# Kernel tuning notes

Hardware: AMD Instinct MI355X
Metric: run time of the kernel (lower is better)

The kernel has to match this reference:

```python
import jax, jax.numpy as jnp
import numpy as np

LN_EPS = 1e-5

def _layernorm(x, g, b):
    mu = jnp.mean(x, axis=-1, keepdims=True)
    var = jnp.var(x, axis=-1, keepdims=True)
    return (x - mu) * jax.lax.rsqrt(var + LN_EPS) * g + b

def setup_inputs() -> dict:
    key = jax.random.key(0)
    ks = jax.random.split(key, 8)
    B, N, n, m, a = 4096, 50000, 1024, 16384, 256
    return {
        "x": jax.random.normal(ks[0], (B, n), dtype=jnp.float32),
        "X_data": jax.random.normal(ks[1], (N, n), dtype=jnp.float32),
        "memory_indices": jax.random.randint(ks[2], (m,), 0, N, dtype=jnp.int64)
            if jax.config.jax_enable_x64 else jax.random.randint(ks[2], (m,), 0, N, dtype=jnp.int32),
        "W_q": jax.random.normal(ks[3], (a, n), dtype=jnp.float32) / np.sqrt(n),
        "W_k": jax.random.normal(ks[4], (a, n), dtype=jnp.float32) / np.sqrt(n),
        "W_v": jax.random.normal(ks[5], (n, n), dtype=jnp.float32) / np.sqrt(n),
        "g_q": jnp.ones((a,), jnp.float32), "b_q": jnp.zeros((a,), jnp.float32),
        "g_k": jnp.ones((a,), jnp.float32), "b_k": jnp.zeros((a,), jnp.float32),
        "g_v": jnp.ones((n,), jnp.float32), "b_v": jnp.zeros((n,), jnp.float32),
    }

def reference(x, X_data, memory_indices, W_q, W_k, W_v, g_q, b_q, g_k, b_k, g_v, b_v):
    # Gather memory bank rows: [m, n]
    X_cross = X_data[memory_indices]
    n = x.shape[-1]
    # preprocess(): scalar normalizer so mean row norm ~= sqrt(n) (SAE convention)
    C = jnp.mean(jnp.linalg.norm(X_cross, axis=-1)) / jnp.sqrt(jnp.asarray(n, x.dtype))
    X_cross = X_cross / C
    xs = x / C
    # QKV projections (Linear, no bias) + per-stream LayerNorm
    q = _layernorm(xs @ W_q.T, g_q, b_q)        # [B, a]
    k = _layernorm(X_cross @ W_k.T, g_k, b_k)   # [m, a]
    v = _layernorm(X_cross @ W_v.T, g_v, b_v)   # [m, n]
    # scaled dot-product attention over the memory bank
    scale = 1.0 / np.sqrt(q.shape[-1])
    attn = jax.nn.softmax(jnp.einsum('ba,ma->bm', q, k) * scale, axis=-1)  # [B, m]
    x_hat = attn @ v                             # [B, n]
    return (xs, x_hat, attn, v)
```

## Files before the change

### kernel.cpp

```cpp
#include <hip/hip_runtime.h>
#include <math.h>

typedef _Float16 hlf4 __attribute__((ext_vector_type(4)));
typedef _Float16 hlf8 __attribute__((ext_vector_type(8)));
typedef float f32x4 __attribute__((ext_vector_type(4)));

static __device__ __forceinline__ void gl_lds16(const void* g, void* l) {
    __builtin_amdgcn_global_load_lds(
        (const __attribute__((address_space(1))) unsigned int*)g,
        (__attribute__((address_space(3))) unsigned int*)l, 16, 0, 0);
}

static __device__ __forceinline__ float blk_sum(float v) {
    __shared__ float sm[256];
    int tid = threadIdx.x;
    sm[tid] = v; __syncthreads();
#pragma unroll
    for (int s = 128; s > 0; s >>= 1) {
        if (tid < s) sm[tid] += sm[tid + s];
        __syncthreads();
    }
    float r = sm[0]; __syncthreads();
    return r;
}

static __device__ __forceinline__ float blk_max(float v) {
    __shared__ float sm[256];
    int tid = threadIdx.x;
    sm[tid] = v; __syncthreads();
#pragma unroll
    for (int s = 128; s > 0; s >>= 1) {
        if (tid < s) sm[tid] = fmaxf(sm[tid], sm[tid + s]);
        __syncthreads();
    }
    float r = sm[0]; __syncthreads();
    return r;
}

__global__ __launch_bounds__(256) void k_cinv(
    const float* __restrict__ norms, int m, int n, float* __restrict__ cinv) {
    float s = 0.f;
    for (int i = threadIdx.x; i < m; i += 256) s += norms[i];
    float tot = blk_sum(s);
    if (threadIdx.x == 0) cinv[0] = (float)m * sqrtf((float)n) / tot;
}

__global__ __launch_bounds__(256) void k_scale2(
    const float* __restrict__ x, const float* __restrict__ cinv,
    float* __restrict__ y, _Float16* __restrict__ yh, long long total4) {
    float c = cinv[0];
    long long i = blockIdx.x * 256ll + threadIdx.x;
    long long stride = (long long)gridDim.x * 256ll;
    for (; i < total4; i += stride) {
        float4 v = ((const float4*)x)[i];
        float4 w = {v.x * c, v.y * c, v.z * c, v.w * c};
        ((float4*)y)[i] = w;
        hlf4 o = {(_Float16)v.x, (_Float16)v.y, (_Float16)v.z, (_Float16)v.w};
        ((hlf4*)yh)[i] = o;
    }
}

__global__ __launch_bounds__(256) void k_gather_cvt(
    const float* __restrict__ X, const int* __restrict__ idx,
    _Float16* __restrict__ out, float* __restrict__ norms, int n) {
    long long r = idx[blockIdx.x];
    const float* src = X + r * (long long)n;
    _Float16* dst = out + (long long)blockIdx.x * n;
    float s = 0.f;
    for (int k = threadIdx.x * 4; k < n; k += 256 * 4) {
        float4 v = *(const float4*)(src + k);
        hlf4 o = {(_Float16)v.x, (_Float16)v.y, (_Float16)v.z, (_Float16)v.w};
        *(hlf4*)(dst + k) = o;
        s = fmaf(v.x, v.x, s); s = fmaf(v.y, v.y, s);
        s = fmaf(v.z, v.z, s); s = fmaf(v.w, v.w, s);
    }
    float tot = blk_sum(s);
    if (threadIdx.x == 0) norms[blockIdx.x] = sqrtf(tot);
}

__global__ __launch_bounds__(256) void k_cvt(
    const float* __restrict__ in, _Float16* __restrict__ out, long long n4,
    float sc) {
    long long i = blockIdx.x * 256ll + threadIdx.x;
    long long stride = (long long)gridDim.x * 256ll;
    for (; i < n4; i += stride) {
        float4 v = ((const float4*)in)[i];
        hlf4 o = {(_Float16)(v.x * sc), (_Float16)(v.y * sc),
                  (_Float16)(v.z * sc), (_Float16)(v.w * sc)};
        ((hlf4*)out)[i] = o;
    }
}

__global__ __launch_bounds__(256) void k_tcvt(
    const float* __restrict__ in, _Float16* __restrict__ out, int R, int Cc) {
    __shared__ _Float16 t[32][34];
    int tx = threadIdx.x & 31, ty = threadIdx.x >> 5;
    int c0 = blockIdx.x * 32, r0 = blockIdx.y * 32;
#pragma unroll
    for (int i = 0; i < 32; i += 8)
        t[ty + i][tx] = (_Float16)in[(long long)(r0 + ty + i) * Cc + c0 + tx];
    __syncthreads();
#pragma unroll
    for (int i = 0; i < 32; i += 8)
        out[(long long)(c0 + ty + i) * R + r0 + tx] = t[tx][ty + i];
}

template <int MODE>
__global__ __launch_bounds__(256) void k_gemm4(
    const _Float16* __restrict__ A, int lda,
    const _Float16* __restrict__ B, int ldb,
    void* __restrict__ Cc, long long ldc, int K,
    float* __restrict__ part, long long zstride) {
    __shared__ _Float16 Ah[2][4096];
    __shared__ _Float16 Bh[2][4096];
    const int tid = threadIdx.x;

    const int gx = gridDim.x, gy = gridDim.y;
    int lin = blockIdx.x + gx * (blockIdx.y + gy * blockIdx.z);
    const int cpx = (gx * gy * (int)gridDim.z) >> 3;
    lin = (lin & 7) * cpx + (lin >> 3);
    const int by = lin % gy;
    const int rest = lin / gy;
    const int bx = rest % gx, bz = rest / gx;

    const long long m0 = (long long)bx * 128;
    const long long n0 = (long long)by * 128;
    const int KC = K / gridDim.z;
    const int kbase = bz * KC;
    const int lane = tid & 63, wv = tid >> 6;
    const int wm = (wv >> 1) * 64, wn = (wv & 1) * 64;
    const int fr = lane & 15, fq = lane >> 4;

    const int s0 = tid, s1 = tid + 256;
    const int r0s = s0 >> 2, r1s = s1 >> 2;
    const int g0 = (((s0 & 3) ^ (r0s & 3)) << 3);
    const int g1 = (((s1 & 3) ^ (r1s & 3)) << 3);
    const _Float16* A0 = A + (m0 + r0s) * (long long)lda + kbase + g0;
    const _Float16* A1 = A + (m0 + r1s) * (long long)lda + kbase + g1;
    const _Float16* B0 = B + (n0 + r0s) * (long long)ldb + kbase + g0;
    const _Float16* B1 = B + (n0 + r1s) * (long long)ldb + kbase + g1;

    f32x4 acc[4][4] = {};

    const int NT = KC / 32;
    {
        gl_lds16(A0, &Ah[0][wv * 512]);
        gl_lds16(A1, &Ah[0][2048 + wv * 512]);
        gl_lds16(B0, &Bh[0][wv * 512]);
        gl_lds16(B1, &Bh[0][2048 + wv * 512]);
    }
    __syncthreads();

    for (int kt = 0; kt < NT; ++kt) {
        const int cur = kt & 1;
        if (kt + 1 < NT) {
            const int nx = cur ^ 1;
            const long long ko = (long long)(kt + 1) * 32;
            gl_lds16(A0 + ko, &Ah[nx][wv * 512]);
            gl_lds16(A1 + ko, &Ah[nx][2048 + wv * 512]);
            gl_lds16(B0 + ko, &Bh[nx][wv * 512]);
            gl_lds16(B1 + ko, &Bh[nx][2048 + wv * 512]);
        }
        hlf8 af[4], bf[4];
#pragma unroll
        for (int i = 0; i < 4; ++i) {
            const int r = wm + i * 16 + fr;
            af[i] = *(const hlf8*)&Ah[cur][r * 32 + ((fq ^ (r & 3)) << 3)];
        }
#pragma unroll
        for (int j = 0; j < 4; ++j) {
            const int r = wn + j * 16 + fr;
            bf[j] = *(const hlf8*)&Bh[cur][r * 32 + ((fq ^ (r & 3)) << 3)];
        }
#pragma unroll
        for (int i = 0; i < 4; ++i)
#pragma unroll
            for (int j = 0; j < 4; ++j)
                acc[i][j] = __builtin_amdgcn_mfma_f32_16x16x32_f16(af[i], bf[j], acc[i][j], 0, 0, 0);
        __syncthreads();
    }

    if constexpr (MODE == 1) {
        _Float16* op = (_Float16*)Cc;
#pragma unroll
        for (int i = 0; i < 4; ++i)
#pragma unroll
            for (int j = 0; j < 4; ++j) {
                _Float16* cp = op + (m0 + wm + i * 16 + fq * 4) * ldc + (n0 + wn + j * 16 + fr);
#pragma unroll
                for (int r = 0; r < 4; ++r)
                    cp[(long long)r * ldc] = (_Float16)__expf(acc[i][j][r] - 5.0f);
            }
    } else {
        float* outp = (gridDim.z == 1) ? (float*)Cc : (part + (long long)bz * zstride);
#pragma unroll
        for (int i = 0; i < 4; ++i)
#pragma unroll
            for (int j = 0; j < 4; ++j) {
                float* cp = outp + (m0 + wm + i * 16 + fq * 4) * ldc + (n0 + wn + j * 16 + fr);
#pragma unroll
                for (int r = 0; r < 4; ++r) cp[(long long)r * ldc] = acc[i][j][r];
            }
    }
}

__global__ __launch_bounds__(256) void k_redux(
    const float* __restrict__ part, float* __restrict__ out,
    long long n4, long long zs4, int Z,
    const float* __restrict__ invs, int rowdiv4) {
    long long i = blockIdx.x * 256ll + threadIdx.x;
    long long stride = (long long)gridDim.x * 256ll;
    for (; i < n4; i += stride) {
        float4 s = ((const float4*)part)[i];
        for (int z = 1; z < Z; ++z) {
            float4 t = ((const float4*)part)[i + z * zs4];
            s.x += t.x; s.y += t.y; s.z += t.z; s.w += t.w;
        }
        if (invs) {
            float iv = invs[i / rowdiv4];
            s.x *= iv; s.y *= iv; s.z *= iv; s.w *= iv;
        }
        ((float4*)out)[i] = s;
    }
}

template <int CNT>
__global__ __launch_bounds__(256) void k_layernorm(
    float* __restrict__ Y, const float* __restrict__ g,
    const float* __restrict__ b, int W) {
    float* yr = Y + (long long)blockIdx.x * W;
    float v[CNT];
    float s = 0.f;
#pragma unroll
    for (int i = 0; i < CNT; ++i) {
        v[i] = yr[threadIdx.x + (i << 8)];
        s += v[i];
    }
    float mu = blk_sum(s) / (float)W;
    float sq = 0.f;
#pragma unroll
    for (int i = 0; i < CNT; ++i) {
        float d = v[i] - mu;
        sq = fmaf(d, d, sq);
    }
    float var = blk_sum(sq) / (float)W;
    float rs = rsqrtf(var + 1e-5f);
#pragma unroll
    for (int i = 0; i < CNT; ++i) {
        int col = threadIdx.x + (i << 8);
        yr[col] = (v[i] - mu) * rs * g[col] + b[col];
    }
}

__global__ __launch_bounds__(256) void k_layernorm_h(
    const float* __restrict__ Y, const float* __restrict__ g,
    const float* __restrict__ b, _Float16* __restrict__ outh, int W, float sc) {
    const float* yr = Y + (long long)blockIdx.x * W;
    _Float16* orow = outh + (long long)blockIdx.x * W;
    float v = yr[threadIdx.x];
    float mu = blk_sum(v) / (float)W;
    float d = v - mu;
    float var = blk_sum(d * d) / (float)W;
    float rs = rsqrtf(var + 1e-5f);
    orow[threadIdx.x] = (_Float16)((d * rs * g[threadIdx.x] + b[threadIdx.x]) * sc);
}

__global__ __launch_bounds__(256) void k_softmax_e(
    const _Float16* __restrict__ E, float* __restrict__ attnf,
    float* __restrict__ invs) {
    const _Float16* er = E + (long long)blockIdx.x * 16384;
    float* ar = attnf + (long long)blockIdx.x * 16384;
    float4 r[16];
    float sum = 0.f;
#pragma unroll
    for (int i = 0; i < 16; ++i) {
        hlf4 h = ((const hlf4*)er)[threadIdx.x + (i << 8)];
        float4 t = {(float)h[0], (float)h[1], (float)h[2], (float)h[3]};
        r[i] = t;
        sum += t.x + t.y + t.z + t.w;
    }
    sum = blk_sum(sum);
    float inv = 1.0f / sum;
    if (threadIdx.x == 0) invs[blockIdx.x] = inv;
#pragma unroll
    for (int i = 0; i < 16; ++i) {
        float4 t = r[i];
        t.x *= inv; t.y *= inv; t.z *= inv; t.w *= inv;
        ((float4*)ar)[threadIdx.x + (i << 8)] = t;
    }
}

extern "C" void kernel_launch(void* const* d_in, const int* in_sizes, int n_in,
                              void* d_out, int out_size, void* d_ws, size_t ws_size,
                              hipStream_t stream) {
    const float* x      = (const float*)d_in[0];
    const float* X_data = (const float*)d_in[1];
    const int*   midx   = (const int*)d_in[2];
    const float* W_q    = (const float*)d_in[3];
    const float* W_k    = (const float*)d_in[4];
    const float* W_v    = (const float*)d_in[5];
    const float* g_q    = (const float*)d_in[6];
    const float* b_q    = (const float*)d_in[7];
    const float* g_k    = (const float*)d_in[8];
    const float* b_k    = (const float*)d_in[9];
    const float* g_v    = (const float*)d_in[10];
    const float* b_v    = (const float*)d_in[11];

    const int n  = in_sizes[10];
    const int a  = in_sizes[6];
    const int m  = in_sizes[2];
    const int Bn = in_sizes[0] / n;

    float* out  = (float*)d_out;
    float* xs   = out;
    float* xhat = xs + (long long)Bn * n;
    float* attn = xhat + (long long)Bn * n;
    float* vout = attn + (long long)Bn * m;

    char* wp = (char*)d_ws;
    auto carve = [&](size_t bytes) -> char* {
        char* r = wp; wp += (bytes + 255) & ~(size_t)255; return r;
    };
    float*     norms = (float*)carve((size_t)m * 4);
    float*     cinv  = (float*)carve(16);
    float*     invs  = (float*)carve((size_t)Bn * 4);
    char*      alias0 = wp;
    float*     qmat  = (float*)carve((size_t)Bn * a * 4);
    float*     kmat  = (float*)carve((size_t)m * a * 4);
    _Float16*  xs_h  = (_Float16*)carve((size_t)Bn * n * 2);
    _Float16*  Xc_h  = (_Float16*)carve((size_t)m * n * 2);
    _Float16*  Wq_h  = (_Float16*)carve((size_t)a * n * 2);
    _Float16*  Wk_h  = (_Float16*)carve((size_t)a * n * 2);
    _Float16*  Wv_h  = (_Float16*)carve((size_t)n * n * 2);
    _Float16*  q_h   = (_Float16*)carve((size_t)Bn * a * 2);
    _Float16*  k_h   = (_Float16*)carve((size_t)m * a * 2);
    float*     splitk = (float*)alias0;
    const int  SK = 4;
    _Float16*  vT_h  = (_Float16*)carve((size_t)n * m * 2);
    size_t used = (size_t)(wp - (char*)d_ws);
    _Float16* attn_h = nullptr;
    if (ws_size >= used + (size_t)Bn * m * 2 + 256)
        attn_h = (_Float16*)carve((size_t)Bn * m * 2);

    hipLaunchKernelGGL(k_gather_cvt, dim3(m), dim3(256), 0, stream,
                       X_data, midx, Xc_h, norms, n);
    hipLaunchKernelGGL(k_cinv, dim3(1), dim3(256), 0, stream, norms, m, n, cinv);

    hipLaunchKernelGGL(k_scale2, dim3(2048), dim3(256), 0, stream,
                       x, cinv, xs, xs_h, (long long)Bn * n / 4);

    hipLaunchKernelGGL(k_cvt, dim3(256), dim3(256), 0, stream, W_q, Wq_h, (long long)a * n / 4, 1.f);
    hipLaunchKernelGGL(k_cvt, dim3(256), dim3(256), 0, stream, W_k, Wk_h, (long long)a * n / 4, 1.f);
    hipLaunchKernelGGL(k_cvt, dim3(1024), dim3(256), 0, stream, W_v, Wv_h, (long long)n * n / 4, 1.f);

    hipLaunchKernelGGL((k_gemm4<0>), dim3(Bn / 128, a / 128), dim3(256), 0, stream,
                       xs_h, n, Wq_h, n, qmat, a, n, (float*)nullptr, 0ll);
    hipLaunchKernelGGL((k_gemm4<0>), dim3(m / 128, a / 128), dim3(256), 0, stream,
                       Xc_h, n, Wk_h, n, kmat, a, n, (float*)nullptr, 0ll);
    hipLaunchKernelGGL((k_gemm4<0>), dim3(m / 128, n / 128), dim3(256), 0, stream,
                       Xc_h, n, Wv_h, n, vout, n, n, (float*)nullptr, 0ll);

    float sc = 1.0f / sqrtf((float)a);
    hipLaunchKernelGGL(k_layernorm_h, dim3(Bn), dim3(256), 0, stream,
                       qmat, g_q, b_q, q_h, a, sc);
    hipLaunchKernelGGL(k_layernorm_h, dim3(m), dim3(256), 0, stream,
                       kmat, g_k, b_k, k_h, a, 1.f);
    hipLaunchKernelGGL(k_layernorm<4>, dim3(m), dim3(256), 0, stream, vout, g_v, b_v, n);
    hipLaunchKernelGGL(k_tcvt, dim3(n / 32, m / 32), dim3(256), 0, stream, vout, vT_h, m, n);

    long long zstride = (long long)Bn * n;
    if (attn_h) {
        hipLaunchKernelGGL((k_gemm4<1>), dim3(Bn / 128, m / 128), dim3(256), 0, stream,
                           q_h, a, k_h, a, attn_h, m, a, (float*)nullptr, 0ll);
        hipLaunchKernelGGL(k_softmax_e, dim3(Bn), dim3(256), 0, stream,
                           attn_h, attn, invs);
        hipLaunchKernelGGL((k_gemm4<0>), dim3(Bn / 128, n / 128, SK), dim3(256), 0, stream,
                           attn_h, m, vT_h, m, xhat, n, m, splitk, zstride);
        hipLaunchKernelGGL(k_redux, dim3(2048), dim3(256), 0, stream,
                           splitk, xhat, (long long)Bn * n / 4, zstride / 4, SK,
                           invs, n / 4);
    } else {
        _Float16* chunk_h = (_Float16*)splitk;
        for (int cb = 0; cb < 4; ++cb) {
            hipLaunchKernelGGL((k_gemm4<1>), dim3(1024 / 128, m / 128), dim3(256), 0, stream,
                               q_h + (long long)cb * 1024 * a, a, k_h, a,
                               chunk_h, m, a, (float*)nullptr, 0ll);
            hipLaunchKernelGGL(k_softmax_e, dim3(1024), dim3(256), 0, stream,
                               chunk_h, attn + (long long)cb * 1024 * m,
                               invs + (long long)cb * 1024);
            hipLaunchKernelGGL((k_gemm4<0>), dim3(1024 / 128, n / 128), dim3(256), 0, stream,
                               chunk_h, m, vT_h, m, xhat + (long long)cb * 1024 * n, n, m,
                               (float*)nullptr, 0ll);
        }
        hipLaunchKernelGGL(k_redux, dim3(2048), dim3(256), 0, stream,
                           xhat, xhat, (long long)Bn * n / 4, 0ll, 1, invs, n / 4);
    }
}
```

Measured before the change: 552.4 us.

## Add 256x256 tile GEMM with 8 waves and interleaved staged prefetch

Adds a new 512-thread GEMM kernel with 256x256 output tiles and a K-step of 64. It uses a wider XOR swizzle and splits each k-step into four quadrant MFMA phases, with half-tile global-to-LDS prefetches interleaved between them and explicit waitcnt, barrier and setprio control. The kernel replaces the 128x128 GEMM for the V projection, the QK^T/exp stage and the split-K attn@V stage, which raises data reuse per block and overlaps loads with MFMA work. The older kernel is cut down to a plain fp32-output version for the small Q/K projections. The new kernel uses 128 KB of LDS and large accumulators, which limits occupancy and gives fewer blocks on the smaller grids.

Result: no change. 561.6 us (+1.7%).

```diff
diff --git a/kernel.cpp b/kernel.cpp
--- a/kernel.cpp
+++ b/kernel.cpp
@@ -18,19 +18,6 @@
 #pragma unroll
     for (int s = 128; s > 0; s >>= 1) {
         if (tid < s) sm[tid] += sm[tid + s];
-        __syncthreads();
-    }
-    float r = sm[0]; __syncthreads();
-    return r;
-}
-
-static __device__ __forceinline__ float blk_max(float v) {
-    __shared__ float sm[256];
-    int tid = threadIdx.x;
-    sm[tid] = v; __syncthreads();
-#pragma unroll
-    for (int s = 128; s > 0; s >>= 1) {
-        if (tid < s) sm[tid] = fmaxf(sm[tid], sm[tid + s]);
         __syncthreads();
     }
     float r = sm[0]; __syncthreads();
@@ -105,28 +92,21 @@
         out[(long long)(c0 + ty + i) * R + r0 + tx] = t[tx][ty + i];
 }
 
-template <int MODE>
 __global__ __launch_bounds__(256) void k_gemm4(
     const _Float16* __restrict__ A, int lda,
     const _Float16* __restrict__ B, int ldb,
-    void* __restrict__ Cc, long long ldc, int K,
-    float* __restrict__ part, long long zstride) {
+    float* __restrict__ Cc, long long ldc, int K) {
     __shared__ _Float16 Ah[2][4096];
     __shared__ _Float16 Bh[2][4096];
     const int tid = threadIdx.x;
-
     const int gx = gridDim.x, gy = gridDim.y;
-    int lin = blockIdx.x + gx * (blockIdx.y + gy * blockIdx.z);
-    const int cpx = (gx * gy * (int)gridDim.z) >> 3;
+    int lin = blockIdx.x + gx * blockIdx.y;
+    const int cpx = (gx * gy) >> 3;
     lin = (lin & 7) * cpx + (lin >> 3);
     const int by = lin % gy;
-    const int rest = lin / gy;
-    const int bx = rest % gx, bz = rest / gx;
-
+    const int bx = lin / gy;
     const long long m0 = (long long)bx * 128;
     const long long n0 = (long long)by * 128;
-    const int KC = K / gridDim.z;
-    const int kbase = bz * KC;
     const int lane = tid & 63, wv = tid >> 6;
     const int wm = (wv >> 1) * 64, wn = (wv & 1) * 64;
     const int fr = lane & 15, fq = lane >> 4;
@@ -135,14 +115,14 @@
     const int r0s = s0 >> 2, r1s = s1 >> 2;
     const int g0 = (((s0 & 3) ^ (r0s & 3)) << 3);
     const int g1 = (((s1 & 3) ^ (r1s & 3)) << 3);
-    const _Float16* A0 = A + (m0 + r0s) * (long long)lda + kbase + g0;
-    const _Float16* A1 = A + (m0 + r1s) * (long long)lda + kbase + g1;
-    const _Float16* B0 = B + (n0 + r0s) * (long long)ldb + kbase + g0;
-    const _Float16* B1 = B + (n0 + r1s) * (long long)ldb + kbase + g1;
+    const _Float16* A0 = A + (m0 + r0s) * (long long)lda + g0;
+    const _Float16* A1 = A + (m0 + r1s) * (long long)lda + g1;
+    const _Float16* B0 = B + (n0 + r0s) * (long long)ldb + g0;
+    const _Float16* B1 = B + (n0 + r1s) * (long long)ldb + g1;
 
     f32x4 acc[4][4] = {};
 
-    const int NT = KC / 32;
+    const int NT = K / 32;
     {
         gl_lds16(A0, &Ah[0][wv * 512]);
         gl_lds16(A1, &Ah[0][2048 + wv * 512]);
@@ -180,10 +160,163 @@
         __syncthreads();
     }
 
+#pragma unroll
+    for (int i = 0; i < 4; ++i)
+#pragma unroll
+        for (int j = 0; j < 4; ++j) {
+            float* cp = Cc + (m0 + wm + i * 16 + fq * 4) * ldc + (n0 + wn + j * 16 + fr);
+#pragma unroll
+            for (int r = 0; r < 4; ++r) cp[(long long)r * ldc] = acc[i][j][r];
+        }
+}
+
+template <int MODE>
+__global__ __launch_bounds__(512) void k256(
+    const _Float16* __restrict__ A, int lda,
+    const _Float16* __restrict__ B, int ldb,
+    void* __restrict__ Cc, long long ldc, int K,
+    float* __restrict__ part, long long zstride) {
+    __shared__ _Float16 Ah[2][16384];
+    __shared__ _Float16 Bh[2][16384];
+    const int tid = threadIdx.x, lane = tid & 63, wv = tid >> 6;
+
+    const int gx = gridDim.x, gy = gridDim.y;
+    int lin = blockIdx.x + gx * (blockIdx.y + gy * blockIdx.z);
+    const int cpx = (gx * gy * (int)gridDim.z) >> 3;
+    lin = (lin & 7) * cpx + (lin >> 3);
+    const int by = lin % gy;
+    const int rest = lin / gy;
+    const int bx = rest % gx, bz = rest / gx;
+
+    const long long m0 = (long long)bx * 256;
+    const long long n0 = (long long)by * 256;
+    const int KC = K / gridDim.z;
+    const int kbase = bz * KC;
+    const int wm = (wv >> 2) * 128, wn = (wv & 3) * 64;
+    const int fr = lane & 15, fq = lane >> 4;
+
+    const int sa = tid, sb = tid + 512;
+    const int ra = sa >> 3, ga = (((sa & 7) ^ (ra & 7)) << 3);
+    const int rb = sb >> 3, gb = (((sb & 7) ^ (rb & 7)) << 3);
+    const _Float16* As0 = A + (m0 + ra) * (long long)lda + kbase + ga;
+    const _Float16* As1 = A + (m0 + rb) * (long long)lda + kbase + gb;
+    const _Float16* Bs0 = B + (n0 + ra) * (long long)ldb + kbase + ga;
+    const _Float16* Bs1 = B + (n0 + rb) * (long long)ldb + kbase + gb;
+
+    f32x4 acc[8][4] = {};
+    const int NT = KC / 64;
+
+#define STG(s0p, s1p, ldm, larr, bufi, h, kt)                                  \
+    {                                                                          \
+        const long long o_ = (long long)(kt) * 64 + (long long)(h) * 128 * (ldm); \
+        gl_lds16((s0p) + o_, &larr[bufi][((h) * 1024 + wv * 64) * 8]);         \
+        gl_lds16((s1p) + o_, &larr[bufi][((h) * 1024 + 512 + wv * 64) * 8]);   \
+    }
+
+    STG(Bs0, Bs1, ldb, Bh, 0, 0, 0);
+    STG(As0, As1, lda, Ah, 0, 0, 0);
+    STG(Bs0, Bs1, ldb, Bh, 0, 1, 0);
+    STG(As0, As1, lda, Ah, 0, 1, 0);
+    STG(Bs0, Bs1, ldb, Bh, 1, 0, 1);
+    STG(As0, As1, lda, Ah, 1, 0, 1);
+
+    for (int kt = 0; kt < NT; ++kt) {
+        const int cur = kt & 1;
+        if (kt + 1 < NT) asm volatile("s_waitcnt vmcnt(4)" ::: "memory");
+        else             asm volatile("s_waitcnt vmcnt(0)" ::: "memory");
+        __builtin_amdgcn_s_barrier();
+
+        hlf8 a0[4][2], a1[4][2], b0[2][2], b1[2][2];
+        if (kt + 1 < NT) STG(Bs0, Bs1, ldb, Bh, cur ^ 1, 1, kt + 1);
+#pragma unroll
+        for (int i = 0; i < 4; ++i)
+#pragma unroll
+            for (int ks = 0; ks < 2; ++ks) {
+                const int rr = wm + i * 16 + fr;
+                a0[i][ks] = *(const hlf8*)&Ah[cur][rr * 64 + (((ks * 4 + fq) ^ (rr & 7)) << 3)];
+            }
+#pragma unroll
+        for (int jj = 0; jj < 2; ++jj)
+#pragma unroll
+            for (int ks = 0; ks < 2; ++ks) {
+                const int cc = wn + jj * 16 + fr;
+                b0[jj][ks] = *(const hlf8*)&Bh[cur][cc * 64 + (((ks * 4 + fq) ^ (cc & 7)) << 3)];
+            }
+        __builtin_amdgcn_s_barrier();
+        asm volatile("s_waitcnt lgkmcnt(0)" ::: "memory");
+        __builtin_amdgcn_sched_barrier(0);
+        __builtin_amdgcn_s_setprio(1);
+#pragma unroll
+        for (int i = 0; i < 4; ++i)
+#pragma unroll
+            for (int jj = 0; jj < 2; ++jj)
+#pragma unroll
+                for (int ks = 0; ks < 2; ++ks)
+                    acc[i][jj] = __builtin_amdgcn_mfma_f32_16x16x32_f16(a0[i][ks], b0[jj][ks], acc[i][jj], 0, 0, 0);
+        __builtin_amdgcn_s_setprio(0);
+        __builtin_amdgcn_s_barrier();
+
+        if (kt + 1 < NT) STG(As0, As1, lda, Ah, cur ^ 1, 1, kt + 1);
+#pragma unroll
+        for (int jj = 0; jj < 2; ++jj)
+#pragma unroll
+            for (int ks = 0; ks < 2; ++ks) {
+                const int cc = wn + (jj + 2) * 16 + fr;
+                b1[jj][ks] = *(const hlf8*)&Bh[cur][cc * 64 + (((ks * 4 + fq) ^ (cc & 7)) << 3)];
+            }
+        __builtin_amdgcn_s_barrier();
+        asm volatile("s_waitcnt lgkmcnt(0)" ::: "memory");
+        __builtin_amdgcn_sched_barrier(0);
+        __builtin_amdgcn_s_setprio(1);
+#pragma unroll
+        for (int i = 0; i < 4; ++i)
+#pragma unroll
+            for (int jj = 0; jj < 2; ++jj)
+#pragma unroll
+                for (int ks = 0; ks < 2; ++ks)
+                    acc[i][jj + 2] = __builtin_amdgcn_mfma_f32_16x16x32_f16(a0[i][ks], b1[jj][ks], acc[i][jj + 2], 0, 0, 0);
+        __builtin_amdgcn_s_setprio(0);
+        __builtin_amdgcn_s_barrier();
+
+        if (kt + 2 < NT) STG(Bs0, Bs1, ldb, Bh, cur, 0, kt + 2);
+#pragma unroll
+        for (int i = 0; i < 4; ++i)
+#pragma unroll
+            for (int ks = 0; ks < 2; ++ks) {
+                const int rr = wm + (i + 4) * 16 + fr;
+                a1[i][ks] = *(const hlf8*)&Ah[cur][rr * 64 + (((ks * 4 + fq) ^ (rr & 7)) << 3)];
+            }
+        __builtin_amdgcn_s_barrier();
+        asm volatile("s_waitcnt lgkmcnt(0)" ::: "memory");
+        __builtin_amdgcn_sched_barrier(0);
+        __builtin_amdgcn_s_setprio(1);
+#pragma unroll
+        for (int i = 0; i < 4; ++i)
+#pragma unroll
+            for (int jj = 0; jj < 2; ++jj)
+#pragma unroll
+                for (int ks = 0; ks < 2; ++ks)
+                    acc[i + 4][jj] = __builtin_amdgcn_mfma_f32_16x16x32_f16(a1[i][ks], b0[jj][ks], acc[i + 4][jj], 0, 0, 0);
+        __builtin_amdgcn_s_setprio(0);
+        __builtin_amdgcn_s_barrier();
+
+        if (kt + 2 < NT) STG(As0, As1, lda, Ah, cur, 0, kt + 2);
+        __builtin_amdgcn_s_setprio(1);
+#pragma unroll
+        for (int i = 0; i < 4; ++i)
+#pragma unroll
+            for (int jj = 0; jj < 2; ++jj)
+#pragma unroll
+                for (int ks = 0; ks < 2; ++ks)
+                    acc[i + 4][jj + 2] = __builtin_amdgcn_mfma_f32_16x16x32_f16(a1[i][ks], b1[jj][ks], acc[i + 4][jj + 2], 0, 0, 0);
+        __builtin_amdgcn_s_setprio(0);
+    }
+#undef STG
+
     if constexpr (MODE == 1) {
         _Float16* op = (_Float16*)Cc;
 #pragma unroll
-        for (int i = 0; i < 4; ++i)
+        for (int i = 0; i < 8; ++i)
 #pragma unroll
             for (int j = 0; j < 4; ++j) {
                 _Float16* cp = op + (m0 + wm + i * 16 + fq * 4) * ldc + (n0 + wn + j * 16 + fr);
@@ -194,7 +327,7 @@
     } else {
         float* outp = (gridDim.z == 1) ? (float*)Cc : (part + (long long)bz * zstride);
 #pragma unroll
-        for (int i = 0; i < 4; ++i)
+        for (int i = 0; i < 8; ++i)
 #pragma unroll
             for (int j = 0; j < 4; ++j) {
                 float* cp = outp + (m0 + wm + i * 16 + fq * 4) * ldc + (n0 + wn + j * 16 + fr);
@@ -353,11 +486,11 @@
     hipLaunchKernelGGL(k_cvt, dim3(256), dim3(256), 0, stream, W_k, Wk_h, (long long)a * n / 4, 1.f);
     hipLaunchKernelGGL(k_cvt, dim3(1024), dim3(256), 0, stream, W_v, Wv_h, (long long)n * n / 4, 1.f);
 
-    hipLaunchKernelGGL((k_gemm4<0>), dim3(Bn / 128, a / 128), dim3(256), 0, stream,
-                       xs_h, n, Wq_h, n, qmat, a, n, (float*)nullptr, 0ll);
-    hipLaunchKernelGGL((k_gemm4<0>), dim3(m / 128, a / 128), dim3(256), 0, stream,
-                       Xc_h, n, Wk_h, n, kmat, a, n, (float*)nullptr, 0ll);
-    hipLaunchKernelGGL((k_gemm4<0>), dim3(m / 128, n / 128), dim3(256), 0, stream,
+    hipLaunchKernelGGL(k_gemm4, dim3(Bn / 128, a / 128), dim3(256), 0, stream,
+                       xs_h, n, Wq_h, n, qmat, a, n);
+    hipLaunchKernelGGL(k_gemm4, dim3(m / 128, a / 128), dim3(256), 0, stream,
+                       Xc_h, n, Wk_h, n, kmat, a, n);
+    hipLaunchKernelGGL((k256<0>), dim3(m / 256, n / 256), dim3(512), 0, stream,
                        Xc_h, n, Wv_h, n, vout, n, n, (float*)nullptr, 0ll);
 
     float sc = 1.0f / sqrtf((float)a);
@@ -370,11 +503,11 @@
 
     long long zstride = (long long)Bn * n;
     if (attn_h) {
-        hipLaunchKernelGGL((k_gemm4<1>), dim3(Bn / 128, m / 128), dim3(256), 0, stream,
+        hipLaunchKernelGGL((k256<1>), dim3(Bn / 256, m / 256), dim3(512), 0, stream,
                            q_h, a, k_h, a, attn_h, m, a, (float*)nullptr, 0ll);
         hipLaunchKernelGGL(k_softmax_e, dim3(Bn), dim3(256), 0, stream,
                            attn_h, attn, invs);
-        hipLaunchKernelGGL((k_gemm4<0>), dim3(Bn / 128, n / 128, SK), dim3(256), 0, stream,
+        hipLaunchKernelGGL((k256<0>), dim3(Bn / 256, n / 256, SK), dim3(512), 0, stream,
                            attn_h, m, vT_h, m, xhat, n, m, splitk, zstride);
         hipLaunchKernelGGL(k_redux, dim3(2048), dim3(256), 0, stream,
                            splitk, xhat, (long long)Bn * n / 4, zstride / 4, SK,
@@ -382,13 +515,13 @@
     } else {
         _Float16* chunk_h = (_Float16*)splitk;
         for (int cb = 0; cb < 4; ++cb) {
-            hipLaunchKernelGGL((k_gemm4<1>), dim3(1024 / 128, m / 128), dim3(256), 0, stream,
+            hipLaunchKernelGGL((k256<1>), dim3(1024 / 256, m / 256), dim3(512), 0, stream,
                                q_h + (long long)cb * 1024 * a, a, k_h, a,
                                chunk_h, m, a, (float*)nullptr, 0ll);
             hipLaunchKernelGGL(k_softmax_e, dim3(1024), dim3(256), 0, stream,
                                chunk_h, attn + (long long)cb * 1024 * m,
                                invs + (long long)cb * 1024);
-            hipLaunchKernelGGL((k_gemm4<0>), dim3(1024 / 128, n / 128), dim3(256), 0, stream,
+            hipLaunchKernelGGL((k256<0>), dim3(1024 / 256, n / 256), dim3(512), 0, stream,
                                chunk_h, m, vT_h, m, xhat + (long long)cb * 1024 * n, n, m,
                                (float*)nullptr, 0ll);
         }
```
